# Kernel optimization log

Hardware: AMD Instinct MI355X
Metric: run time of the kernel (lower is better)

## Reference

```python
import jax, jax.numpy as jnp
import numpy as np

T, B, L, I, H = 1024, 1024, 10, 10, 10


def setup_inputs() -> dict:
    key = jax.random.key(0)
    ks = jax.random.split(key, 7)
    scale = 1.0 / np.sqrt(H)
    x = jax.random.normal(ks[0], (T, B, I), dtype=jnp.float32)
    hp = jax.random.normal(ks[1], (L, B, H), dtype=jnp.float32)
    cp = jax.random.normal(ks[2], (L, B, H), dtype=jnp.float32)
    # torch nn.LSTM params, uniform(-1/sqrt(H), 1/sqrt(H)); layer 0 input = I == H so all layers stack
    W_ih = jax.random.uniform(ks[3], (L, 4 * H, I), minval=-scale, maxval=scale, dtype=jnp.float32)
    W_hh = jax.random.uniform(ks[4], (L, 4 * H, H), minval=-scale, maxval=scale, dtype=jnp.float32)
    b_ih = jax.random.uniform(ks[5], (L, 4 * H), minval=-scale, maxval=scale, dtype=jnp.float32)
    b_hh = jax.random.uniform(ks[6], (L, 4 * H), minval=-scale, maxval=scale, dtype=jnp.float32)
    return {"x": x, "hp": hp, "cp": cp, "W_ih": W_ih, "W_hh": W_hh, "b_ih": b_ih, "b_hh": b_hh}


def _run_layer(inp, h0, c0, Wi, Wh, bi, bh):
    # precompute input projections for all timesteps: [T, B, 4H]
    xg = jnp.einsum('tbi,gi->tbg', inp, Wi) + bi + bh

    def step(carry, xg_t):
        h, c = carry
        g = xg_t + h @ Wh.T  # [B, 4H]; torch gate order: i, f, g, o
        i_g, f_g, g_g, o_g = jnp.split(g, 4, axis=-1)
        i_g = jax.nn.sigmoid(i_g)
        f_g = jax.nn.sigmoid(f_g)
        g_g = jnp.tanh(g_g)
        o_g = jax.nn.sigmoid(o_g)
        c = f_g * c + i_g * g_g
        h = o_g * jnp.tanh(c)
        return (h, c), h

    (hT, cT), ys = jax.lax.scan(step, (h0, c0), xg)
    return ys, hT, cT


def reference(x, hp, cp, W_ih, W_hh, b_ih, b_hh):
    out = x
    hns, cns = [], []
    for l in range(hp.shape[0]):  # fixed small layer stack
        out, hn, cn = _run_layer(out, hp[l], cp[l], W_ih[l], W_hh[l], b_ih[l], b_hh[l])
        hns.append(hn)
        cns.append(cn)
    return out, jnp.stack(hns), jnp.stack(cns)
```

## Files before the change

kernel.cpp:

```cpp
#include <hip/hip_runtime.h>

namespace {

constexpr int T = 1024;
constexpr int B = 1024;
constexpr int L = 10;
constexpr int H = 10;
constexpr int NTHREADS = 128;
constexpr int U = 4;
constexpr int NWIN = T / U;
constexpr int NINT = NWIN + L - 1;
constexpr int BH = B * H;
constexpr int ROWF = 20;

using v2f = __attribute__((ext_vector_type(2))) float;
using v4f = __attribute__((ext_vector_type(4))) float;

__device__ __forceinline__ v2f v2fma(v2f a, v2f b, v2f c) {
    return __builtin_elementwise_fma(a, b, c);
}
__device__ __forceinline__ void pin2(v2f& v) { asm volatile("" : "+v"(v)); }
__device__ __forceinline__ float rcp_f(float x) { return __builtin_amdgcn_rcpf(x); }
__device__ __forceinline__ float exp2_f(float x) {
    float r; asm("v_exp_f32 %0, %1" : "=v"(r) : "v"(x)); return r;
}
__device__ __forceinline__ v2f lo2(v4f q) { return __builtin_shufflevector(q, q, 0, 1); }
__device__ __forceinline__ v2f hi2(v4f q) { return __builtin_shufflevector(q, q, 2, 3); }

__global__
__attribute__((amdgpu_flat_work_group_size(NTHREADS, NTHREADS)))
__attribute__((amdgpu_waves_per_eu(2)))
void lstm_pipeline(const float* __restrict__ x,
                   const float* __restrict__ hp,
                   const float* __restrict__ cp,
                   const float* __restrict__ Wih,
                   const float* __restrict__ Whh,
                   const float* __restrict__ bih,
                   const float* __restrict__ bhh,
                   float* __restrict__ out,
                   float* __restrict__ hn,
                   float* __restrict__ cn)
{
    __shared__ __align__(16) float buf[2][U][L + 1][ROWF];

    const int tid = threadIdx.x;
    const int wv = tid >> 6;
    const int ln = tid & 63;
    int lidx;
    if (wv == 0) lidx = (ln < 60) ? ln : (ln - 10);
    else         lidx = (ln < 40) ? (60 + ln) : (90 + (ln - 40) % 10);
    const int l = lidx / 10;
    const int j = lidx % 10;
    const int b = blockIdx.x;
    const int boff = b * H + j;

    const float NL2E = -1.44269504088896340736f;
    v2f sA; sA[0] = NL2E;        sA[1] = NL2E;
    v2f sB; sB[0] = 2.0f * NL2E; sB[1] = NL2E;
    v2f wiA[10], wiB[10], whA[10], whB[10], bA, bB;
    {
        const float* WiL = Wih + (size_t)l * 4 * H * H;
        const float* WhL = Whh + (size_t)l * 4 * H * H;
        #pragma unroll
        for (int k = 0; k < 10; ++k) {
            v2f t;
            t[0] = WiL[(0 * H + j) * H + k]; t[1] = WiL[(1 * H + j) * H + k];
            wiA[k] = t * sA;
            t[0] = WiL[(2 * H + j) * H + k]; t[1] = WiL[(3 * H + j) * H + k];
            wiB[k] = t * sB;
            t[0] = WhL[(0 * H + j) * H + k]; t[1] = WhL[(1 * H + j) * H + k];
            whA[k] = t * sA;
            t[0] = WhL[(2 * H + j) * H + k]; t[1] = WhL[(3 * H + j) * H + k];
            whB[k] = t * sB;
        }
        const int bo = l * 4 * H;
        bA[0] = bih[bo + j] + bhh[bo + j];
        bA[1] = bih[bo + H + j] + bhh[bo + H + j];
        bB[0] = bih[bo + 2 * H + j] + bhh[bo + 2 * H + j];
        bB[1] = bih[bo + 3 * H + j] + bhh[bo + 3 * H + j];
        bA = bA * sA;
        bB = bB * sB;
    }
    #pragma unroll
    for (int k = 0; k < 10; ++k) { pin2(wiA[k]); pin2(wiB[k]); pin2(whA[k]); pin2(whB[k]); }
    pin2(bA); pin2(bB);

    float h = hp[(l * B + b) * H + j];
    float c = cp[(l * B + b) * H + j];
    {
        v2f hh; hh[0] = h; hh[1] = h;
        *(v2f*)&buf[(l + 1) & 1][U - 1][l + 1][2 * j] = hh;
    }

    const bool is_st = (lidx < 10);
    float xcur[U], xnext[U];
    if (is_st) {
        #pragma unroll
        for (int u = 0; u < U; ++u) {
            float xv = x[(size_t)u * BH + boff];
            v2f xx; xx[0] = xv; xx[1] = xv;
            *(v2f*)&buf[1][u][0][2 * j] = xx;
        }
        #pragma unroll
        for (int u = 0; u < U; ++u) xcur[u] = x[(size_t)(U + u) * BH + boff];
    }
    __syncthreads();

    auto interval = [&](int k, int wp, int rp) {
        if (is_st && (k + 2) < NWIN) {
            #pragma unroll
            for (int u = 0; u < U; ++u)
                xnext[u] = x[(size_t)((k + 2) * U + u) * BH + boff];
        }
        const unsigned w = (unsigned)(k - l);
        if (w < (unsigned)NWIN) {
            v4f hq0 = *(const v4f*)&buf[rp][U - 1][l + 1][0];
            v4f hq1 = *(const v4f*)&buf[rp][U - 1][l + 1][4];
            v4f hq2 = *(const v4f*)&buf[rp][U - 1][l + 1][8];
            v4f hq3 = *(const v4f*)&buf[rp][U - 1][l + 1][12];
            v4f hq4 = *(const v4f*)&buf[rp][U - 1][l + 1][16];
            v2f aA[U], aB[U];
            #pragma unroll
            for (int u = 0; u < U; ++u) {
                const float* xr = &buf[rp][u][l][0];
                v4f q0 = *(const v4f*)(xr + 0);
                v4f q1 = *(const v4f*)(xr + 4);
                v4f q2 = *(const v4f*)(xr + 8);
                v4f q3 = *(const v4f*)(xr + 12);
                v4f q4 = *(const v4f*)(xr + 16);
                v2f a1 = v2fma(wiA[0], lo2(q0), bA);
                v2f a2 = wiA[1] * hi2(q0);
                v2f b1 = v2fma(wiB[0], lo2(q0), bB);
                v2f b2 = wiB[1] * hi2(q0);
                a1 = v2fma(wiA[2], lo2(q1), a1);  a2 = v2fma(wiA[3], hi2(q1), a2);
                b1 = v2fma(wiB[2], lo2(q1), b1);  b2 = v2fma(wiB[3], hi2(q1), b2);
                a1 = v2fma(wiA[4], lo2(q2), a1);  a2 = v2fma(wiA[5], hi2(q2), a2);
                b1 = v2fma(wiB[4], lo2(q2), b1);  b2 = v2fma(wiB[5], hi2(q2), b2);
                a1 = v2fma(wiA[6], lo2(q3), a1);  a2 = v2fma(wiA[7], hi2(q3), a2);
                b1 = v2fma(wiB[6], lo2(q3), b1);  b2 = v2fma(wiB[7], hi2(q3), b2);
                a1 = v2fma(wiA[8], lo2(q4), a1);  a2 = v2fma(wiA[9], hi2(q4), a2);
                b1 = v2fma(wiB[8], lo2(q4), b1);  b2 = v2fma(wiB[9], hi2(q4), b2);
                aA[u] = a1 + a2;
                aB[u] = b1 + b2;
            }
            float hv[U];
            #pragma unroll
            for (int u = 0; u < U; ++u) {
                v4f q0, q1, q2, q3, q4;
                if (u == 0) { q0 = hq0; q1 = hq1; q2 = hq2; q3 = hq3; q4 = hq4; }
                else {
                    const float* hr = &buf[wp][u - 1][l + 1][0];
                    q0 = *(const v4f*)(hr + 0);
                    q1 = *(const v4f*)(hr + 4);
                    q2 = *(const v4f*)(hr + 8);
                    q3 = *(const v4f*)(hr + 12);
                    q4 = *(const v4f*)(hr + 16);
                }
                v2f a1 = v2fma(whA[0], lo2(q0), aA[u]);
                v2f a2 = whA[1] * hi2(q0);
                v2f b1 = v2fma(whB[0], lo2(q0), aB[u]);
                v2f b2 = whB[1] * hi2(q0);
                a1 = v2fma(whA[2], lo2(q1), a1);  a2 = v2fma(whA[3], hi2(q1), a2);
                b1 = v2fma(whB[2], lo2(q1), b1);  b2 = v2fma(whB[3], hi2(q1), b2);
                a1 = v2fma(whA[4], lo2(q2), a1);  a2 = v2fma(whA[5], hi2(q2), a2);
                b1 = v2fma(whB[4], lo2(q2), b1);  b2 = v2fma(whB[5], hi2(q2), b2);
                a1 = v2fma(whA[6], lo2(q3), a1);  a2 = v2fma(whA[7], hi2(q3), a2);
                b1 = v2fma(whB[6], lo2(q3), b1);  b2 = v2fma(whB[7], hi2(q3), b2);
                a1 = v2fma(whA[8], lo2(q4), a1);  a2 = v2fma(whA[9], hi2(q4), a2);
                b1 = v2fma(whB[8], lo2(q4), b1);  b2 = v2fma(whB[9], hi2(q4), b2);
                const v2f pA = a1 + a2;
                const v2f pB = b1 + b2;
                const float Ei = exp2_f(pA[0]);
                const float Ef = exp2_f(pA[1]);
                const float Eg = exp2_f(pB[0]);
                const float Eo = exp2_f(pB[1]);
                const float d1 = 1.0f + Ef;
                const float e1 = 1.0f + Ei;
                const float e2 = 1.0f + Eg;
                const float d2 = e1 * e2;
                const float num = fmaf(c, d2, (1.0f - Eg) * d1);
                c = num * rcp_f(d1 * d2);
                const float Ec = exp2_f((2.0f * NL2E) * c);
                const float o1 = 1.0f + Eo;
                const float o2 = 1.0f + Ec;
                h = (1.0f - Ec) * rcp_f(o1 * o2);
                v2f hh; hh[0] = h; hh[1] = h;
                *(v2f*)&buf[wp][u][l + 1][2 * j] = hh;
                hv[u] = h;
            }
            if (l == L - 1) {
                const int t0 = (int)w * U;
                #pragma unroll
                for (int u = 0; u < U; ++u)
                    out[(size_t)(t0 + u) * BH + boff] = hv[u];
            }
        }
        if (is_st && (k + 1) < NWIN) {
            #pragma unroll
            for (int u = 0; u < U; ++u) {
                v2f xx; xx[0] = xcur[u]; xx[1] = xcur[u];
                *(v2f*)&buf[wp][u][0][2 * j] = xx;
            }
            #pragma unroll
            for (int u = 0; u < U; ++u) xcur[u] = xnext[u];
        }
        __syncthreads();
    };

    for (int kk = 0; kk < NINT + 1; kk += 2) {
        interval(kk, 0, 1);
        interval(kk + 1, 1, 0);
    }

    hn[(l * B + b) * H + j] = h;
    cn[(l * B + b) * H + j] = c;
}

}

extern "C" void kernel_launch(void* const* d_in, const int* in_sizes, int n_in,
                              void* d_out, int out_size, void* d_ws, size_t ws_size,
                              hipStream_t stream) {
    (void)in_sizes; (void)n_in; (void)d_ws; (void)ws_size; (void)out_size;
    const float* x   = (const float*)d_in[0];
    const float* hp  = (const float*)d_in[1];
    const float* cp  = (const float*)d_in[2];
    const float* Wih = (const float*)d_in[3];
    const float* Whh = (const float*)d_in[4];
    const float* bih = (const float*)d_in[5];
    const float* bhh = (const float*)d_in[6];

    float* out = (float*)d_out;
    float* hn  = out + (size_t)T * B * H;
    float* cn  = hn + (size_t)L * B * H;

    lstm_pipeline<<<dim3(B), dim3(NTHREADS), 0, stream>>>(
        x, hp, cp, Wih, Whh, bih, bhh, out, hn, cn);
}
```

Measured before the change: 488.0 us.

## Skew second wave by a phase so input projection overlaps recurrent step

Splits each interval into a prefetch, an input-projection phase, a recurrent phase and an x-staging phase. Wave 0 keeps the original order, while the other wave runs the recurrent phase of the previous interval before the input projection of the current one, so the two waves do different kinds of work between barriers. The input-projection FMA chains are also collapsed from two split accumulators into one longer serial chain. The skewed schedule depends on LDS double-buffer timing across waves. The longer dependency chain could cost latency.

```diff
diff --git a/kernel.cpp b/kernel.cpp
--- a/kernel.cpp
+++ b/kernel.cpp
@@ -26,6 +26,7 @@
 }
 __device__ __forceinline__ v2f lo2(v4f q) { return __builtin_shufflevector(q, q, 0, 1); }
 __device__ __forceinline__ v2f hi2(v4f q) { return __builtin_shufflevector(q, q, 2, 3); }
+#define LDS_FENCE asm volatile("" ::: "memory")
 
 __global__
 __attribute__((amdgpu_flat_work_group_size(NTHREADS, NTHREADS)))
@@ -106,12 +107,45 @@
     }
     __syncthreads();
 
-    auto interval = [&](int k, int wp, int rp) {
+    v2f aA[U], aB[U];
+
+    auto prefetchx = [&](int k) {
         if (is_st && (k + 2) < NWIN) {
             #pragma unroll
             for (int u = 0; u < U; ++u)
                 xnext[u] = x[(size_t)((k + 2) * U + u) * BH + boff];
         }
+    };
+
+    auto phase1 = [&](int k, int rp) {
+        const unsigned w = (unsigned)(k - l);
+        if (w < (unsigned)NWIN) {
+            #pragma unroll
+            for (int u = 0; u < U; ++u) {
+                const float* xr = &buf[rp][u][l][0];
+                v4f q0 = *(const v4f*)(xr + 0);
+                v4f q1 = *(const v4f*)(xr + 4);
+                v4f q2 = *(const v4f*)(xr + 8);
+                v4f q3 = *(const v4f*)(xr + 12);
+                v4f q4 = *(const v4f*)(xr + 16);
+                v2f a  = v2fma(wiA[0], lo2(q0), bA);
+                v2f bv = v2fma(wiB[0], lo2(q0), bB);
+                a = v2fma(wiA[1], hi2(q0), a);  bv = v2fma(wiB[1], hi2(q0), bv);
+                a = v2fma(wiA[2], lo2(q1), a);  bv = v2fma(wiB[2], lo2(q1), bv);
+                a = v2fma(wiA[3], hi2(q1), a);  bv = v2fma(wiB[3], hi2(q1), bv);
+                a = v2fma(wiA[4], lo2(q2), a);  bv = v2fma(wiB[4], lo2(q2), bv);
+                a = v2fma(wiA[5], hi2(q2), a);  bv = v2fma(wiB[5], hi2(q2), bv);
+                a = v2fma(wiA[6], lo2(q3), a);  bv = v2fma(wiB[6], lo2(q3), bv);
+                a = v2fma(wiA[7], hi2(q3), a);  bv = v2fma(wiB[7], hi2(q3), bv);
+                a = v2fma(wiA[8], lo2(q4), a);  bv = v2fma(wiB[8], lo2(q4), bv);
+                a = v2fma(wiA[9], hi2(q4), a);  bv = v2fma(wiB[9], hi2(q4), bv);
+                aA[u] = a;
+                aB[u] = bv;
+            }
+        }
+    };
+
+    auto phase2 = [&](int k, int wp, int rp) {
         const unsigned w = (unsigned)(k - l);
         if (w < (unsigned)NWIN) {
             v4f hq0 = *(const v4f*)&buf[rp][U - 1][l + 1][0];
@@ -119,30 +153,6 @@
             v4f hq2 = *(const v4f*)&buf[rp][U - 1][l + 1][8];
             v4f hq3 = *(const v4f*)&buf[rp][U - 1][l + 1][12];
             v4f hq4 = *(const v4f*)&buf[rp][U - 1][l + 1][16];
-            v2f aA[U], aB[U];
-            #pragma unroll
-            for (int u = 0; u < U; ++u) {
-                const float* xr = &buf[rp][u][l][0];
-                v4f q0 = *(const v4f*)(xr + 0);
-                v4f q1 = *(const v4f*)(xr + 4);
-                v4f q2 = *(const v4f*)(xr + 8);
-                v4f q3 = *(const v4f*)(xr + 12);
-                v4f q4 = *(const v4f*)(xr + 16);
-                v2f a1 = v2fma(wiA[0], lo2(q0), bA);
-                v2f a2 = wiA[1] * hi2(q0);
-                v2f b1 = v2fma(wiB[0], lo2(q0), bB);
-                v2f b2 = wiB[1] * hi2(q0);
-                a1 = v2fma(wiA[2], lo2(q1), a1);  a2 = v2fma(wiA[3], hi2(q1), a2);
-                b1 = v2fma(wiB[2], lo2(q1), b1);  b2 = v2fma(wiB[3], hi2(q1), b2);
-                a1 = v2fma(wiA[4], lo2(q2), a1);  a2 = v2fma(wiA[5], hi2(q2), a2);
-                b1 = v2fma(wiB[4], lo2(q2), b1);  b2 = v2fma(wiB[5], hi2(q2), b2);
-                a1 = v2fma(wiA[6], lo2(q3), a1);  a2 = v2fma(wiA[7], hi2(q3), a2);
-                b1 = v2fma(wiB[6], lo2(q3), b1);  b2 = v2fma(wiB[7], hi2(q3), b2);
-                a1 = v2fma(wiA[8], lo2(q4), a1);  a2 = v2fma(wiA[9], hi2(q4), a2);
-                b1 = v2fma(wiB[8], lo2(q4), b1);  b2 = v2fma(wiB[9], hi2(q4), b2);
-                aA[u] = a1 + a2;
-                aB[u] = b1 + b2;
-            }
             float hv[U];
             #pragma unroll
             for (int u = 0; u < U; ++u) {
@@ -195,6 +205,9 @@
                     out[(size_t)(t0 + u) * BH + boff] = hv[u];
             }
         }
+    };
+
+    auto stagex = [&](int k, int wp) {
         if (is_st && (k + 1) < NWIN) {
             #pragma unroll
             for (int u = 0; u < U; ++u) {
@@ -204,12 +217,30 @@
             #pragma unroll
             for (int u = 0; u < U; ++u) xcur[u] = xnext[u];
         }
-        __syncthreads();
-    };
-
-    for (int kk = 0; kk < NINT + 1; kk += 2) {
-        interval(kk, 0, 1);
-        interval(kk + 1, 1, 0);
+    };
+
+    if (wv == 0) {
+        for (int kk = 0; kk < NINT + 1; kk += 2) {
+            prefetchx(kk);
+            phase1(kk, 1);        LDS_FENCE;
+            phase2(kk, 0, 1);     LDS_FENCE;
+            stagex(kk, 0);
+            __syncthreads();
+            prefetchx(kk + 1);
+            phase1(kk + 1, 0);    LDS_FENCE;
+            phase2(kk + 1, 1, 0); LDS_FENCE;
+            stagex(kk + 1, 1);
+            __syncthreads();
+        }
+    } else {
+        for (int kk = 0; kk < NINT + 1; kk += 2) {
+            phase2(kk - 1, 1, 0); LDS_FENCE;
+            phase1(kk, 1);
+            __syncthreads();
+            phase2(kk, 0, 1);     LDS_FENCE;
+            phase1(kk + 1, 0);
+            __syncthreads();
+        }
     }
 
     hn[(l * B + b) * H + j] = h;
```

Result: no change. 484.5 us (-0.7%).

## Split LSTM block into producer waves for input projection and consumer waves for recurrence

Applied to the files above, without the earlier changes.

Doubles the workgroup to four waves. Two producer waves compute the input-to-hidden gate projections into a shared-memory buffer, and two consumer waves run the recurrent part from that buffer. The layer wavefront schedule is stretched to two intervals per layer so the two roles overlap across double-buffered rows. This takes the input-projection FMAs off the serial recurrent critical path and halves per-thread weight registers. In exchange it adds shared-memory traffic, a longer pipeline fill, and more waves per block.

```diff
diff --git a/kernel.cpp b/kernel.cpp
--- a/kernel.cpp
+++ b/kernel.cpp
@@ -6,12 +6,13 @@
 constexpr int B = 1024;
 constexpr int L = 10;
 constexpr int H = 10;
-constexpr int NTHREADS = 128;
+constexpr int NTHREADS = 256;
 constexpr int U = 4;
 constexpr int NWIN = T / U;
-constexpr int NINT = NWIN + L - 1;
+constexpr int NINT2 = 2 * (L - 1) + NWIN + 2;
 constexpr int BH = B * H;
 constexpr int ROWF = 20;
+constexpr int NITEM = 100;
 
 using v2f = __attribute__((ext_vector_type(2))) float;
 using v4f = __attribute__((ext_vector_type(4))) float;
@@ -29,7 +30,7 @@
 
 __global__
 __attribute__((amdgpu_flat_work_group_size(NTHREADS, NTHREADS)))
-__attribute__((amdgpu_waves_per_eu(2)))
+__attribute__((amdgpu_waves_per_eu(4)))
 void lstm_pipeline(const float* __restrict__ x,
                    const float* __restrict__ hp,
                    const float* __restrict__ cp,
@@ -41,10 +42,13 @@
                    float* __restrict__ hn,
                    float* __restrict__ cn)
 {
-    __shared__ __align__(16) float buf[2][U][L + 1][ROWF];
+    __shared__ __align__(16) float rows[2][U][L + 1][ROWF];
+    __shared__ __align__(16) float abuf[2][U][NITEM][4];
 
     const int tid = threadIdx.x;
-    const int wv = tid >> 6;
+    const int wvraw = tid >> 6;
+    const bool producer = (wvraw >= 2);
+    const int wv = wvraw & 1;
     const int ln = tid & 63;
     int lidx;
     if (wv == 0) lidx = (ln < 60) ? ln : (ln - 10);
@@ -57,21 +61,16 @@
     const float NL2E = -1.44269504088896340736f;
     v2f sA; sA[0] = NL2E;        sA[1] = NL2E;
     v2f sB; sB[0] = 2.0f * NL2E; sB[1] = NL2E;
-    v2f wiA[10], wiB[10], whA[10], whB[10], bA, bB;
-    {
+    v2f wA[10], wB[10], bA, bB;
+    if (producer) {
         const float* WiL = Wih + (size_t)l * 4 * H * H;
-        const float* WhL = Whh + (size_t)l * 4 * H * H;
         #pragma unroll
         for (int k = 0; k < 10; ++k) {
             v2f t;
             t[0] = WiL[(0 * H + j) * H + k]; t[1] = WiL[(1 * H + j) * H + k];
-            wiA[k] = t * sA;
+            wA[k] = t * sA;
             t[0] = WiL[(2 * H + j) * H + k]; t[1] = WiL[(3 * H + j) * H + k];
-            wiB[k] = t * sB;
-            t[0] = WhL[(0 * H + j) * H + k]; t[1] = WhL[(1 * H + j) * H + k];
-            whA[k] = t * sA;
-            t[0] = WhL[(2 * H + j) * H + k]; t[1] = WhL[(3 * H + j) * H + k];
-            whB[k] = t * sB;
+            wB[k] = t * sB;
         }
         const int bo = l * 4 * H;
         bA[0] = bih[bo + j] + bhh[bo + j];
@@ -80,94 +79,125 @@
         bB[1] = bih[bo + 3 * H + j] + bhh[bo + 3 * H + j];
         bA = bA * sA;
         bB = bB * sB;
+    } else {
+        const float* WhL = Whh + (size_t)l * 4 * H * H;
+        #pragma unroll
+        for (int k = 0; k < 10; ++k) {
+            v2f t;
+            t[0] = WhL[(0 * H + j) * H + k]; t[1] = WhL[(1 * H + j) * H + k];
+            wA[k] = t * sA;
+            t[0] = WhL[(2 * H + j) * H + k]; t[1] = WhL[(3 * H + j) * H + k];
+            wB[k] = t * sB;
+        }
+        bA[0] = 0.0f; bA[1] = 0.0f; bB = bA;
     }
     #pragma unroll
-    for (int k = 0; k < 10; ++k) { pin2(wiA[k]); pin2(wiB[k]); pin2(whA[k]); pin2(whB[k]); }
+    for (int k = 0; k < 10; ++k) { pin2(wA[k]); pin2(wB[k]); }
     pin2(bA); pin2(bB);
 
-    float h = hp[(l * B + b) * H + j];
-    float c = cp[(l * B + b) * H + j];
-    {
+    float h = 0.0f, c = 0.0f;
+    if (!producer) {
+        h = hp[(l * B + b) * H + j];
+        c = cp[(l * B + b) * H + j];
         v2f hh; hh[0] = h; hh[1] = h;
-        *(v2f*)&buf[(l + 1) & 1][U - 1][l + 1][2 * j] = hh;
-    }
-
-    const bool is_st = (lidx < 10);
+        *(v2f*)&rows[0][U - 1][l + 1][2 * j] = hh;
+    }
+
+    const bool is_st = producer && (wv == 0) && (ln < 10);
     float xcur[U], xnext[U];
     if (is_st) {
         #pragma unroll
         for (int u = 0; u < U; ++u) {
             float xv = x[(size_t)u * BH + boff];
             v2f xx; xx[0] = xv; xx[1] = xv;
-            *(v2f*)&buf[1][u][0][2 * j] = xx;
+            *(v2f*)&rows[1][u][0][2 * j] = xx;
         }
         #pragma unroll
         for (int u = 0; u < U; ++u) xcur[u] = x[(size_t)(U + u) * BH + boff];
     }
     __syncthreads();
 
-    auto interval = [&](int k, int wp, int rp) {
+    auto prod = [&](int k, int pk) {
         if (is_st && (k + 2) < NWIN) {
             #pragma unroll
             for (int u = 0; u < U; ++u)
                 xnext[u] = x[(size_t)((k + 2) * U + u) * BH + boff];
         }
-        const unsigned w = (unsigned)(k - l);
+        const unsigned w = (unsigned)(k - 2 * l);
         if (w < (unsigned)NWIN) {
-            v4f hq0 = *(const v4f*)&buf[rp][U - 1][l + 1][0];
-            v4f hq1 = *(const v4f*)&buf[rp][U - 1][l + 1][4];
-            v4f hq2 = *(const v4f*)&buf[rp][U - 1][l + 1][8];
-            v4f hq3 = *(const v4f*)&buf[rp][U - 1][l + 1][12];
-            v4f hq4 = *(const v4f*)&buf[rp][U - 1][l + 1][16];
-            v2f aA[U], aB[U];
             #pragma unroll
             for (int u = 0; u < U; ++u) {
-                const float* xr = &buf[rp][u][l][0];
+                const float* xr = &rows[pk ^ 1][u][l][0];
                 v4f q0 = *(const v4f*)(xr + 0);
                 v4f q1 = *(const v4f*)(xr + 4);
                 v4f q2 = *(const v4f*)(xr + 8);
                 v4f q3 = *(const v4f*)(xr + 12);
                 v4f q4 = *(const v4f*)(xr + 16);
-                v2f a1 = v2fma(wiA[0], lo2(q0), bA);
-                v2f a2 = wiA[1] * hi2(q0);
-                v2f b1 = v2fma(wiB[0], lo2(q0), bB);
-                v2f b2 = wiB[1] * hi2(q0);
-                a1 = v2fma(wiA[2], lo2(q1), a1);  a2 = v2fma(wiA[3], hi2(q1), a2);
-                b1 = v2fma(wiB[2], lo2(q1), b1);  b2 = v2fma(wiB[3], hi2(q1), b2);
-                a1 = v2fma(wiA[4], lo2(q2), a1);  a2 = v2fma(wiA[5], hi2(q2), a2);
-                b1 = v2fma(wiB[4], lo2(q2), b1);  b2 = v2fma(wiB[5], hi2(q2), b2);
-                a1 = v2fma(wiA[6], lo2(q3), a1);  a2 = v2fma(wiA[7], hi2(q3), a2);
-                b1 = v2fma(wiB[6], lo2(q3), b1);  b2 = v2fma(wiB[7], hi2(q3), b2);
-                a1 = v2fma(wiA[8], lo2(q4), a1);  a2 = v2fma(wiA[9], hi2(q4), a2);
-                b1 = v2fma(wiB[8], lo2(q4), b1);  b2 = v2fma(wiB[9], hi2(q4), b2);
-                aA[u] = a1 + a2;
-                aB[u] = b1 + b2;
-            }
+                v2f a  = v2fma(wA[0], lo2(q0), bA);
+                v2f bv = v2fma(wB[0], lo2(q0), bB);
+                a = v2fma(wA[1], hi2(q0), a);  bv = v2fma(wB[1], hi2(q0), bv);
+                a = v2fma(wA[2], lo2(q1), a);  bv = v2fma(wB[2], lo2(q1), bv);
+                a = v2fma(wA[3], hi2(q1), a);  bv = v2fma(wB[3], hi2(q1), bv);
+                a = v2fma(wA[4], lo2(q2), a);  bv = v2fma(wB[4], lo2(q2), bv);
+                a = v2fma(wA[5], hi2(q2), a);  bv = v2fma(wB[5], hi2(q2), bv);
+                a = v2fma(wA[6], lo2(q3), a);  bv = v2fma(wB[6], lo2(q3), bv);
+                a = v2fma(wA[7], hi2(q3), a);  bv = v2fma(wB[7], hi2(q3), bv);
+                a = v2fma(wA[8], lo2(q4), a);  bv = v2fma(wB[8], lo2(q4), bv);
+                a = v2fma(wA[9], hi2(q4), a);  bv = v2fma(wB[9], hi2(q4), bv);
+                v4f o = __builtin_shufflevector(a, bv, 0, 1, 2, 3);
+                *(v4f*)&abuf[pk][u][lidx][0] = o;
+            }
+        }
+        if (is_st && (k + 1) < NWIN) {
+            #pragma unroll
+            for (int u = 0; u < U; ++u) {
+                v2f xx; xx[0] = xcur[u]; xx[1] = xcur[u];
+                *(v2f*)&rows[pk][u][0][2 * j] = xx;
+            }
+            #pragma unroll
+            for (int u = 0; u < U; ++u) xcur[u] = xnext[u];
+        }
+    };
+
+    auto cons = [&](int k, int pk) {
+        const unsigned w = (unsigned)(k - 2 * l - 1);
+        if (w < (unsigned)NWIN) {
+            const float* hr0 = &rows[pk ^ 1][U - 1][l + 1][0];
+            v4f hq0 = *(const v4f*)(hr0 + 0);
+            v4f hq1 = *(const v4f*)(hr0 + 4);
+            v4f hq2 = *(const v4f*)(hr0 + 8);
+            v4f hq3 = *(const v4f*)(hr0 + 12);
+            v4f hq4 = *(const v4f*)(hr0 + 16);
+            v4f av0 = *(const v4f*)&abuf[pk ^ 1][0][lidx][0];
+            v4f av1 = *(const v4f*)&abuf[pk ^ 1][1][lidx][0];
+            v4f av2 = *(const v4f*)&abuf[pk ^ 1][2][lidx][0];
+            v4f av3 = *(const v4f*)&abuf[pk ^ 1][3][lidx][0];
             float hv[U];
             #pragma unroll
             for (int u = 0; u < U; ++u) {
                 v4f q0, q1, q2, q3, q4;
                 if (u == 0) { q0 = hq0; q1 = hq1; q2 = hq2; q3 = hq3; q4 = hq4; }
                 else {
-                    const float* hr = &buf[wp][u - 1][l + 1][0];
+                    const float* hr = &rows[pk][u - 1][l + 1][0];
                     q0 = *(const v4f*)(hr + 0);
                     q1 = *(const v4f*)(hr + 4);
                     q2 = *(const v4f*)(hr + 8);
                     q3 = *(const v4f*)(hr + 12);
                     q4 = *(const v4f*)(hr + 16);
                 }
-                v2f a1 = v2fma(whA[0], lo2(q0), aA[u]);
-                v2f a2 = whA[1] * hi2(q0);
-                v2f b1 = v2fma(whB[0], lo2(q0), aB[u]);
-                v2f b2 = whB[1] * hi2(q0);
-                a1 = v2fma(whA[2], lo2(q1), a1);  a2 = v2fma(whA[3], hi2(q1), a2);
-                b1 = v2fma(whB[2], lo2(q1), b1);  b2 = v2fma(whB[3], hi2(q1), b2);
-                a1 = v2fma(whA[4], lo2(q2), a1);  a2 = v2fma(whA[5], hi2(q2), a2);
-                b1 = v2fma(whB[4], lo2(q2), b1);  b2 = v2fma(whB[5], hi2(q2), b2);
-                a1 = v2fma(whA[6], lo2(q3), a1);  a2 = v2fma(whA[7], hi2(q3), a2);
-                b1 = v2fma(whB[6], lo2(q3), b1);  b2 = v2fma(whB[7], hi2(q3), b2);
-                a1 = v2fma(whA[8], lo2(q4), a1);  a2 = v2fma(whA[9], hi2(q4), a2);
-                b1 = v2fma(whB[8], lo2(q4), b1);  b2 = v2fma(whB[9], hi2(q4), b2);
+                v4f av = (u == 0) ? av0 : (u == 1) ? av1 : (u == 2) ? av2 : av3;
+                v2f a1 = v2fma(wA[0], lo2(q0), lo2(av));
+                v2f a2 = wA[1] * hi2(q0);
+                v2f b1 = v2fma(wB[0], lo2(q0), hi2(av));
+                v2f b2 = wB[1] * hi2(q0);
+                a1 = v2fma(wA[2], lo2(q1), a1);  a2 = v2fma(wA[3], hi2(q1), a2);
+                b1 = v2fma(wB[2], lo2(q1), b1);  b2 = v2fma(wB[3], hi2(q1), b2);
+                a1 = v2fma(wA[4], lo2(q2), a1);  a2 = v2fma(wA[5], hi2(q2), a2);
+                b1 = v2fma(wB[4], lo2(q2), b1);  b2 = v2fma(wB[5], hi2(q2), b2);
+                a1 = v2fma(wA[6], lo2(q3), a1);  a2 = v2fma(wA[7], hi2(q3), a2);
+                b1 = v2fma(wB[6], lo2(q3), b1);  b2 = v2fma(wB[7], hi2(q3), b2);
+                a1 = v2fma(wA[8], lo2(q4), a1);  a2 = v2fma(wA[9], hi2(q4), a2);
+                b1 = v2fma(wB[8], lo2(q4), b1);  b2 = v2fma(wB[9], hi2(q4), b2);
                 const v2f pA = a1 + a2;
                 const v2f pB = b1 + b2;
                 const float Ei = exp2_f(pA[0]);
@@ -185,7 +215,7 @@
                 const float o2 = 1.0f + Ec;
                 h = (1.0f - Ec) * rcp_f(o1 * o2);
                 v2f hh; hh[0] = h; hh[1] = h;
-                *(v2f*)&buf[wp][u][l + 1][2 * j] = hh;
+                *(v2f*)&rows[pk][u][l + 1][2 * j] = hh;
                 hv[u] = h;
             }
             if (l == L - 1) {
@@ -195,25 +225,19 @@
                     out[(size_t)(t0 + u) * BH + boff] = hv[u];
             }
         }
-        if (is_st && (k + 1) < NWIN) {
-            #pragma unroll
-            for (int u = 0; u < U; ++u) {
-                v2f xx; xx[0] = xcur[u]; xx[1] = xcur[u];
-                *(v2f*)&buf[wp][u][0][2 * j] = xx;
-            }
-            #pragma unroll
-            for (int u = 0; u < U; ++u) xcur[u] = xnext[u];
-        }
+    };
+
+    for (int kk = 0; kk < NINT2; kk += 2) {
+        if (producer) prod(kk, 0); else cons(kk, 0);
         __syncthreads();
-    };
-
-    for (int kk = 0; kk < NINT + 1; kk += 2) {
-        interval(kk, 0, 1);
-        interval(kk + 1, 1, 0);
-    }
-
-    hn[(l * B + b) * H + j] = h;
-    cn[(l * B + b) * H + j] = c;
+        if (producer) prod(kk + 1, 1); else cons(kk + 1, 1);
+        __syncthreads();
+    }
+
+    if (!producer) {
+        hn[(l * B + b) * H + j] = h;
+        cn[(l * B + b) * H + j] = c;
+    }
 }
 
 }
```

New measurement: 521.6 us. 1.07x slower.
